# Kernel tuning notes

Measured on AMD Instinct MI355X. Metric: run time of the kernel, lower is better.

The kernel has to match this reference:

```python
import jax, jax.numpy as jnp
import numpy as np

N = 131072        # active input voxels (= output voxels for submanifold conv)
KVOL = 27         # 3x3x3 kernel volume
P = 65536         # neighbor pairs per kernel offset (regularized kernel map)
CIN = 64
COUT = 64


def setup_inputs() -> dict:
    key = jax.random.key(0)
    k1, k2, k3, k4, k5 = jax.random.split(key, 5)
    in_feats = jax.random.normal(k1, (N, CIN), dtype=jnp.float32)
    kernel = jax.random.normal(k2, (KVOL, CIN, COUT), dtype=jnp.float32) * (1.0 / np.sqrt(CIN * KVOL))
    bias_param = jax.random.normal(k3, (COUT,), dtype=jnp.float32)
    imap = jax.random.randint(k4, (KVOL, P), 0, N, dtype=jnp.int32)
    omap = jax.random.randint(k5, (KVOL, P), 0, N, dtype=jnp.int32)
    return {"in_feats": in_feats, "kernel": kernel, "bias_param": bias_param,
            "imap": imap, "omap": omap}


def reference(in_feats, kernel, bias_param, imap, omap):
    # Sparse 3D conv as gather -> per-offset GEMM -> scatter-add.
    # gathered: [KVOL, P, CIN]
    gathered = in_feats[imap]
    # per-offset GEMM: [KVOL, P, COUT]
    contrib = jnp.einsum('kpc,kco->kpo', gathered, kernel)
    out = jnp.zeros((N, COUT), dtype=in_feats.dtype)
    out = out.at[omap.reshape(-1)].add(contrib.reshape(-1, COUT))
    out = out + bias_param
    return out
```

## Files before the change

### kernel.cpp

```cpp
#include <hip/hip_runtime.h>
#include <hip/hip_bf16.h>
#include <stdint.h>

#define N_VOX 131072
#define KVOL  27
#define PPK   65536
#define CIN   64
#define COUT  64
#define TOT   (KVOL * PPK)
#define SORT_BLOCKS 864
#define GEMM_BLOCKS (KVOL * (PPK / 128))
#define NBUCKET 256
#define BUCKET_CAP 8192
#define CURSOR_STRIDE 16

typedef __attribute__((ext_vector_type(8))) short short8;
typedef __attribute__((ext_vector_type(4))) float f32x4;

__device__ __forceinline__ void gl_lds16(const void* g, void* l) {
  __builtin_amdgcn_global_load_lds(
      (const __attribute__((address_space(1))) unsigned int*)g,
      (__attribute__((address_space(3))) unsigned int*)l,
      16, 0, 0);
}

__device__ __forceinline__ unsigned short f2bf(float f) {
  __hip_bfloat16 h = __float2bfloat16(f);
  return *reinterpret_cast<unsigned short*>(&h);
}


__global__ __launch_bounds__(256) void prep_sort1_kernel(
    const float* __restrict__ in, unsigned short* __restrict__ inb,
    const float* __restrict__ w, unsigned short* __restrict__ wt,
    const int* __restrict__ omap, unsigned int* __restrict__ cursor,
    unsigned int* __restrict__ pairs, int do_sort) {
  int b = blockIdx.x;
  if (do_sort) {
    if (b < SORT_BLOCKS) {
      __shared__ unsigned int hist[NBUCKET];
      __shared__ unsigned int bbase[NBUCKET];
      int tid = threadIdx.x;
      hist[tid] = 0;
      __syncthreads();
      int e0 = (b * 256 + tid) * 8;
      int4 o0 = *(const int4*)(omap + e0);
      int4 o1 = *(const int4*)(omap + e0 + 4);
      unsigned int k[8] = {(unsigned)o0.x, (unsigned)o0.y, (unsigned)o0.z, (unsigned)o0.w,
                           (unsigned)o1.x, (unsigned)o1.y, (unsigned)o1.z, (unsigned)o1.w};
#pragma unroll
      for (int i = 0; i < 8; i++) atomicAdd(&hist[k[i] >> 9], 1u);
      __syncthreads();
      unsigned int n = hist[tid];
      unsigned int base = n ? atomicAdd(&cursor[tid * CURSOR_STRIDE], n) : 0u;
      bbase[tid] = (unsigned)tid * BUCKET_CAP + base;
      hist[tid] = 0;
      __syncthreads();
#pragma unroll
      for (int i = 0; i < 8; i++) {
        unsigned int bk = k[i] >> 9;
        unsigned int r = atomicAdd(&hist[bk], 1u);
        unsigned int pos = bbase[bk] + r;
        if (pos < (bk + 1) * BUCKET_CAP)
          pairs[pos] = (((unsigned)(e0 + i)) << 9) | (k[i] & 511u);
      }
      return;
    }
    b -= SORT_BLOCKS;
  }
  if (b < 4096) {
    int i = b * 256 + threadIdx.x;
    const float4* in4 = (const float4*)in;
    float4 f0 = in4[2 * i], f1 = in4[2 * i + 1];
    union { unsigned short u[8]; short8 v; } r;
    r.u[0] = f2bf(f0.x); r.u[1] = f2bf(f0.y); r.u[2] = f2bf(f0.z); r.u[3] = f2bf(f0.w);
    r.u[4] = f2bf(f1.x); r.u[5] = f2bf(f1.y); r.u[6] = f2bf(f1.z); r.u[7] = f2bf(f1.w);
    ((short8*)inb)[i] = r.v;
  } else {
    int k = b - 4096;
    const float* wk = w + k * CIN * COUT;
    unsigned short* wtk = wt + k * CIN * COUT;
    for (int idx = threadIdx.x; idx < CIN * COUT; idx += 256) {
      int c = idx >> 6, o = idx & 63;
      wtk[o * 64 + c] = f2bf(wk[idx]);
    }
  }
}


__global__ __launch_bounds__(512) void sort_pass2_kernel(
    const unsigned int* __restrict__ cursor, const unsigned int* __restrict__ pairs,
    int* __restrict__ islot, int* __restrict__ ofs, int* __restrict__ cnt) {
  __shared__ unsigned int hist[512];
  __shared__ unsigned int binofs[512];
  __shared__ unsigned int csc[512];
  __shared__ unsigned int sb_s, n_s;
  int b = blockIdx.x, tid = threadIdx.x;

  unsigned int cv = (tid < NBUCKET) ? cursor[tid * CURSOR_STRIDE] : 0u;
  csc[tid] = cv;
  __syncthreads();
  for (int off = 1; off < 512; off <<= 1) {
    unsigned int t = (tid >= off) ? csc[tid - off] : 0u;
    __syncthreads();
    csc[tid] += t;
    __syncthreads();
  }
  if (tid == b) {
    sb_s = csc[tid] - cv;
    n_s  = cv > BUCKET_CAP ? BUCKET_CAP : cv;
  }
  hist[tid] = 0;
  __syncthreads();
  unsigned int sb = sb_s, n = n_s;
  const unsigned int* reg = pairs + (size_t)b * BUCKET_CAP;

  for (unsigned int i = tid; i < n; i += 512)
    atomicAdd(&hist[reg[i] & 511u], 1u);
  __syncthreads();

  unsigned int h = hist[tid];
  csc[tid] = h;
  __syncthreads();
  for (int off = 1; off < 512; off <<= 1) {
    unsigned int t = (tid >= off) ? csc[tid - off] : 0u;
    __syncthreads();
    csc[tid] += t;
    __syncthreads();
  }
  binofs[tid] = csc[tid] - h;
  int key = (b << 9) | tid;
  ofs[key] = (int)(sb + binofs[tid]);
  cnt[key] = (int)h;
  __syncthreads();

  for (unsigned int i = tid; i < n; i += 512) {
    unsigned int v = reg[i];
    unsigned int r = atomicAdd(&binofs[v & 511u], 1u);
    islot[v >> 9] = (int)(sb + r);
  }
}


__global__ __launch_bounds__(256) void spconv_store_kernel(
    const unsigned short* __restrict__ inb,
    const unsigned short* __restrict__ wt,
    const int* __restrict__ imap,
    const int* __restrict__ islot,
    unsigned short* __restrict__ contrib) {
  __shared__ __align__(16) char smem[24576];
  short* A_lds = (short*)smem;
  short* B_lds = (short*)(smem + 16384);
  short* C_sh  = (short*)smem;
  __shared__ int perm_s[128];

  int bid = blockIdx.x;
  int k = bid >> 9;
  int pbase = (bid & 511) * 128;
  int tid = threadIdx.x;
  int wave = tid >> 6, lane = tid & 63;
  int m = lane & 15, q = lane >> 4;

  const int* imk = imap + k * PPK;
  const unsigned short* wtk = wt + k * 4096;

  if (tid < 128) perm_s[tid] = islot[k * PPK + pbase + tid];

#pragma unroll
  for (int i = 0; i < 2; i++) {
    int id = wave * 2 + i;
    int t = id >> 1, s = id & 1;
    const unsigned short* g = wtk + (t * 16 + m) * 64 + s * 32 + q * 8;
    gl_lds16(g, &B_lds[(t * 128 + s * 64) * 8]);
  }
#pragma unroll
  for (int j = 0; j < 2; j++) {
    int r = wave * 2 + j;
    int row = imk[pbase + r * 16 + m];
    const unsigned short* g0 = inb + row * 64 + q * 8;
    gl_lds16(g0,      &A_lds[(r * 128)      * 8]);
    gl_lds16(g0 + 32, &A_lds[(r * 128 + 64) * 8]);
  }
  __syncthreads();

  const short8* Af = (const short8*)A_lds;
  const short8* Bf = (const short8*)B_lds;

  short8 a[2][2], b[4][2];
#pragma unroll
  for (int r2 = 0; r2 < 2; r2++) {
    int r = wave * 2 + r2;
#pragma unroll
    for (int s = 0; s < 2; s++) a[r2][s] = Af[r * 128 + s * 64 + lane];
  }
#pragma unroll
  for (int t = 0; t < 4; t++)
#pragma unroll
    for (int s = 0; s < 2; s++) b[t][s] = Bf[t * 128 + s * 64 + lane];

  __syncthreads();

  f32x4 acc[2][4];
#pragma unroll
  for (int r2 = 0; r2 < 2; r2++)
#pragma unroll
    for (int t = 0; t < 4; t++) {
      f32x4 c = {0.f, 0.f, 0.f, 0.f};
      c = __builtin_amdgcn_mfma_f32_16x16x32_bf16(a[r2][0], b[t][0], c, 0, 0, 0);
      c = __builtin_amdgcn_mfma_f32_16x16x32_bf16(a[r2][1], b[t][1], c, 0, 0, 0);
      acc[r2][t] = c;
    }

#pragma unroll
  for (int r2 = 0; r2 < 2; r2++) {
    int pl = (wave * 2 + r2) * 16 + q * 4;
#pragma unroll
    for (int t = 0; t < 4; t++)
#pragma unroll
      for (int reg = 0; reg < 4; reg++)
        C_sh[(pl + reg) * 72 + t * 16 + m] = (short)f2bf(acc[r2][t][reg]);
  }
  __syncthreads();

#pragma unroll
  for (int i = 0; i < 4; i++) {
    int id = i * 256 + tid;
    int row = id >> 3, ch = (id & 7) * 8;
    short8 v = *(const short8*)&C_sh[row * 72 + ch];
    __builtin_nontemporal_store(v, (short8*)&contrib[(size_t)perm_s[row] * 64 + ch]);
  }
}


__global__ __launch_bounds__(256) void reduce_kernel(
    const unsigned short* __restrict__ contrib,
    const int* __restrict__ ofs,
    const int* __restrict__ cnt,
    const float* __restrict__ bias,
    float* __restrict__ out) {
  int row = blockIdx.x * 4 + (threadIdx.x >> 6);
  int lane = threadIdx.x & 63;
  int rg = lane >> 3, ch = (lane & 7) * 8;
  int s = ofs[row], n = cnt[row];

  float acc[8];
#pragma unroll
  for (int i = 0; i < 8; i++) acc[i] = 0.f;

  int j = rg;
  for (; j + 8 < n; j += 16) {
    short8 v0 = __builtin_nontemporal_load((const short8*)&contrib[(size_t)(s + j) * 64 + ch]);
    short8 v1 = __builtin_nontemporal_load((const short8*)&contrib[(size_t)(s + j + 8) * 64 + ch]);
#pragma unroll
    for (int i = 0; i < 8; i++)
      acc[i] += __uint_as_float((unsigned int)(unsigned short)v0[i] << 16);
#pragma unroll
    for (int i = 0; i < 8; i++)
      acc[i] += __uint_as_float((unsigned int)(unsigned short)v1[i] << 16);
  }
  if (j < n) {
    short8 v0 = __builtin_nontemporal_load((const short8*)&contrib[(size_t)(s + j) * 64 + ch]);
#pragma unroll
    for (int i = 0; i < 8; i++)
      acc[i] += __uint_as_float((unsigned int)(unsigned short)v0[i] << 16);
  }

#pragma unroll
  for (int mask = 8; mask < 64; mask <<= 1)
#pragma unroll
    for (int i = 0; i < 8; i++) acc[i] += __shfl_xor(acc[i], mask, 64);

  if (rg == 0) {
    float4 b0 = *(const float4*)(bias + ch);
    float4 b1 = *(const float4*)(bias + ch + 4);
    float4 r0 = {acc[0] + b0.x, acc[1] + b0.y, acc[2] + b0.z, acc[3] + b0.w};
    float4 r1 = {acc[4] + b1.x, acc[5] + b1.y, acc[6] + b1.z, acc[7] + b1.w};
    *(float4*)(out + (size_t)row * 64 + ch) = r0;
    *(float4*)(out + (size_t)row * 64 + ch + 4) = r1;
  }
}


__global__ __launch_bounds__(256) void init_out_kernel(float* __restrict__ out,
                                                       const float* __restrict__ bias) {
  int i = blockIdx.x * blockDim.x + threadIdx.x;
  float4 b = *(const float4*)(bias + ((i * 4) & 63));
  ((float4*)out)[i] = b;
}

__global__ __launch_bounds__(256) void spconv_atomic_kernel(
    const unsigned short* __restrict__ inb,
    const unsigned short* __restrict__ wt,
    const int* __restrict__ imap, const int* __restrict__ omap,
    float* __restrict__ out) {
  __shared__ __align__(16) short A_lds[128 * 64];
  __shared__ __align__(16) short B_lds[64 * 64];

  int bid = blockIdx.x;
  int k = bid >> 9;
  int pbase = (bid & 511) * 128;
  int tid = threadIdx.x;
  int wave = tid >> 6, lane = tid & 63;
  int m = lane & 15, q = lane >> 4;

  const int* imk = imap + k * PPK;
  const int* omk = omap + k * PPK;
  const unsigned short* wtk = wt + k * 4096;

#pragma unroll
  for (int i = 0; i < 2; i++) {
    int id = wave * 2 + i;
    int t = id >> 1, s = id & 1;
    const unsigned short* g = wtk + (t * 16 + m) * 64 + s * 32 + q * 8;
    gl_lds16(g, &B_lds[(t * 128 + s * 64) * 8]);
  }
#pragma unroll
  for (int j = 0; j < 2; j++) {
    int r = wave * 2 + j;
    int row = imk[pbase + r * 16 + m];
    const unsigned short* g0 = inb + row * 64 + q * 8;
    gl_lds16(g0,      &A_lds[(r * 128)      * 8]);
    gl_lds16(g0 + 32, &A_lds[(r * 128 + 64) * 8]);
  }
  __syncthreads();

  const short8* Af = (const short8*)A_lds;
  const short8* Bf = (const short8*)B_lds;
  short8 a[2][2], b[4][2];
#pragma unroll
  for (int r2 = 0; r2 < 2; r2++) {
    int r = wave * 2 + r2;
#pragma unroll
    for (int s = 0; s < 2; s++) a[r2][s] = Af[r * 128 + s * 64 + lane];
  }
#pragma unroll
  for (int t = 0; t < 4; t++)
#pragma unroll
    for (int s = 0; s < 2; s++) b[t][s] = Bf[t * 128 + s * 64 + lane];

  f32x4 acc[2][4];
#pragma unroll
  for (int r2 = 0; r2 < 2; r2++)
#pragma unroll
    for (int t = 0; t < 4; t++) {
      f32x4 c = {0.f, 0.f, 0.f, 0.f};
      c = __builtin_amdgcn_mfma_f32_16x16x32_bf16(a[r2][0], b[t][0], c, 0, 0, 0);
      c = __builtin_amdgcn_mfma_f32_16x16x32_bf16(a[r2][1], b[t][1], c, 0, 0, 0);
      acc[r2][t] = c;
    }

  int orow[2][4];
#pragma unroll
  for (int r2 = 0; r2 < 2; r2++) {
    int pr = pbase + (wave * 2 + r2) * 16 + q * 4;
#pragma unroll
    for (int reg = 0; reg < 4; reg++) orow[r2][reg] = omk[pr + reg];
  }
#pragma unroll
  for (int r2 = 0; r2 < 2; r2++)
#pragma unroll
    for (int t = 0; t < 4; t++)
#pragma unroll
      for (int reg = 0; reg < 4; reg++)
        atomicAdd(out + (size_t)orow[r2][reg] * 64 + t * 16 + m, acc[r2][t][reg]);
}


extern "C" void kernel_launch(void* const* d_in, const int* in_sizes, int n_in,
                              void* d_out, int out_size, void* d_ws, size_t ws_size,
                              hipStream_t stream) {
  const float* in_feats = (const float*)d_in[0];
  const float* kern     = (const float*)d_in[1];
  const float* bias     = (const float*)d_in[2];
  const int*   imap     = (const int*)d_in[3];
  const int*   omap     = (const int*)d_in[4];
  float* out = (float*)d_out;

  char* ws = (char*)d_ws;
  size_t off = 0;
  auto alloc = [&](size_t bytes) { size_t o = off; off = (off + bytes + 255) & ~(size_t)255; return o; };

  size_t o_inb   = alloc((size_t)N_VOX * CIN * 2);
  size_t o_wt    = alloc((size_t)KVOL * CIN * COUT * 2);
  size_t o_cnt   = alloc((size_t)N_VOX * 4);
  size_t o_ofs   = alloc((size_t)N_VOX * 4);
  size_t o_islot = alloc((size_t)TOT * 4);
  size_t o_cur   = alloc((size_t)NBUCKET * CURSOR_STRIDE * 4);
  size_t o_ctb   = alloc((size_t)TOT * 64 * 2);
  size_t needed = off;

  unsigned short* inb = (unsigned short*)(ws + o_inb);
  unsigned short* wt  = (unsigned short*)(ws + o_wt);
  int* cnt   = (int*)(ws + o_cnt);
  int* ofs   = (int*)(ws + o_ofs);
  int* islot = (int*)(ws + o_islot);
  unsigned int* cursor = (unsigned int*)(ws + o_cur);
  unsigned short* ctb = (unsigned short*)(ws + o_ctb);
  unsigned int* pairs = (unsigned int*)(ws + o_ctb);

  bool fast = (ws_size >= needed);

  if (fast) {
    (void)hipMemsetAsync(cursor, 0, (size_t)NBUCKET * CURSOR_STRIDE * 4, stream);
    prep_sort1_kernel<<<SORT_BLOCKS + 4096 + KVOL, 256, 0, stream>>>(
        in_feats, inb, kern, wt, omap, cursor, pairs, 1);
    sort_pass2_kernel<<<NBUCKET, 512, 0, stream>>>(cursor, pairs, islot, ofs, cnt);
    spconv_store_kernel<<<GEMM_BLOCKS, 256, 0, stream>>>(inb, wt, imap, islot, ctb);
    reduce_kernel<<<N_VOX / 4, 256, 0, stream>>>(ctb, ofs, cnt, bias, out);
  } else {
    prep_sort1_kernel<<<4096 + KVOL, 256, 0, stream>>>(
        in_feats, inb, kern, wt, omap, nullptr, nullptr, 0);
    init_out_kernel<<<(N_VOX * COUT / 4) / 256, 256, 0, stream>>>(out, bias);
    spconv_atomic_kernel<<<GEMM_BLOCKS, 256, 0, stream>>>(inb, wt, imap, omap, out);
  }
}
```

Measured before the change: 262.2 us.

## Replace two-pass bucket sort with partial counting sort and LDS-accumulating reduce

Replaces the atomic-cursor bucket sort and the per-voxel segmented second pass with a deterministic three-stage counting sort over 512 coarse buckets: per-block histograms, a scan, then a scatter that writes slot indices plus an 8-bit low key. The reduce now gives each block one 256-voxel bucket and accumulates contributions into a 64 KB LDS tile with shared-memory float atomics. This removes the global cursor atomics, the bucket-capacity limit and the fine-grained sort pass. The cost is extra kernel launches, 64 KB of LDS per reduce block (which limits occupancy), and only 512 reduce blocks.

```diff
diff --git a/kernel.cpp b/kernel.cpp
--- a/kernel.cpp
+++ b/kernel.cpp
@@ -10,9 +10,7 @@
 #define TOT   (KVOL * PPK)
 #define SORT_BLOCKS 864
 #define GEMM_BLOCKS (KVOL * (PPK / 128))
-#define NBUCKET 256
-#define BUCKET_CAP 8192
-#define CURSOR_STRIDE 16
+#define NB    512
 
 typedef __attribute__((ext_vector_type(8))) short short8;
 typedef __attribute__((ext_vector_type(4))) float f32x4;
@@ -30,40 +28,31 @@
 }
 
 
-__global__ __launch_bounds__(256) void prep_sort1_kernel(
+__global__ __launch_bounds__(256) void prep_hist_kernel(
     const float* __restrict__ in, unsigned short* __restrict__ inb,
     const float* __restrict__ w, unsigned short* __restrict__ wt,
-    const int* __restrict__ omap, unsigned int* __restrict__ cursor,
-    unsigned int* __restrict__ pairs, int do_sort) {
+    const int* __restrict__ omap, int* __restrict__ counts, int do_sort) {
   int b = blockIdx.x;
   if (do_sort) {
     if (b < SORT_BLOCKS) {
-      __shared__ unsigned int hist[NBUCKET];
-      __shared__ unsigned int bbase[NBUCKET];
+      __shared__ unsigned int hist[NB];
       int tid = threadIdx.x;
-      hist[tid] = 0;
+      hist[tid] = 0; hist[tid + 256] = 0;
       __syncthreads();
       int e0 = (b * 256 + tid) * 8;
       int4 o0 = *(const int4*)(omap + e0);
       int4 o1 = *(const int4*)(omap + e0 + 4);
-      unsigned int k[8] = {(unsigned)o0.x, (unsigned)o0.y, (unsigned)o0.z, (unsigned)o0.w,
-                           (unsigned)o1.x, (unsigned)o1.y, (unsigned)o1.z, (unsigned)o1.w};
-#pragma unroll
-      for (int i = 0; i < 8; i++) atomicAdd(&hist[k[i] >> 9], 1u);
+      atomicAdd(&hist[(unsigned)o0.x >> 8], 1u);
+      atomicAdd(&hist[(unsigned)o0.y >> 8], 1u);
+      atomicAdd(&hist[(unsigned)o0.z >> 8], 1u);
+      atomicAdd(&hist[(unsigned)o0.w >> 8], 1u);
+      atomicAdd(&hist[(unsigned)o1.x >> 8], 1u);
+      atomicAdd(&hist[(unsigned)o1.y >> 8], 1u);
+      atomicAdd(&hist[(unsigned)o1.z >> 8], 1u);
+      atomicAdd(&hist[(unsigned)o1.w >> 8], 1u);
       __syncthreads();
-      unsigned int n = hist[tid];
-      unsigned int base = n ? atomicAdd(&cursor[tid * CURSOR_STRIDE], n) : 0u;
-      bbase[tid] = (unsigned)tid * BUCKET_CAP + base;
-      hist[tid] = 0;
-      __syncthreads();
-#pragma unroll
-      for (int i = 0; i < 8; i++) {
-        unsigned int bk = k[i] >> 9;
-        unsigned int r = atomicAdd(&hist[bk], 1u);
-        unsigned int pos = bbase[bk] + r;
-        if (pos < (bk + 1) * BUCKET_CAP)
-          pairs[pos] = (((unsigned)(e0 + i)) << 9) | (k[i] & 511u);
-      }
+      counts[(size_t)tid * SORT_BLOCKS + b] = (int)hist[tid];
+      counts[(size_t)(tid + 256) * SORT_BLOCKS + b] = (int)hist[tid + 256];
       return;
     }
     b -= SORT_BLOCKS;
@@ -88,57 +77,80 @@
 }
 
 
-__global__ __launch_bounds__(512) void sort_pass2_kernel(
-    const unsigned int* __restrict__ cursor, const unsigned int* __restrict__ pairs,
-    int* __restrict__ islot, int* __restrict__ ofs, int* __restrict__ cnt) {
-  __shared__ unsigned int hist[512];
-  __shared__ unsigned int binofs[512];
-  __shared__ unsigned int csc[512];
-  __shared__ unsigned int sb_s, n_s;
+__global__ __launch_bounds__(256) void scan_blocks_kernel(
+    const int* __restrict__ counts, int* __restrict__ blockbase,
+    int* __restrict__ totals) {
+  __shared__ int s[256];
+  int b = blockIdx.x, t = threadIdx.x;
+  const int* row = counts + (size_t)b * SORT_BLOCKS;
+  int4 c = make_int4(0, 0, 0, 0);
+  if (t < 216) c = *(const int4*)(row + t * 4);
+  int sum = c.x + c.y + c.z + c.w;
+  s[t] = sum; __syncthreads();
+  for (int off = 1; off < 256; off <<= 1) {
+    int v = (t >= off) ? s[t - off] : 0;
+    __syncthreads();
+    s[t] += v;
+    __syncthreads();
+  }
+  int excl = s[t] - sum;
+  int* brow = blockbase + (size_t)b * SORT_BLOCKS;
+  if (t < 216) {
+    brow[t * 4]     = excl;
+    brow[t * 4 + 1] = excl + c.x;
+    brow[t * 4 + 2] = excl + c.x + c.y;
+    brow[t * 4 + 3] = excl + c.x + c.y + c.z;
+  }
+  if (t == 255) totals[b] = s[255];
+}
+
+
+__global__ __launch_bounds__(NB) void base_kernel(const int* __restrict__ totals,
+                                                  int* __restrict__ bbase) {
+  __shared__ int s[NB];
+  int t = threadIdx.x;
+  int v = totals[t];
+  s[t] = v; __syncthreads();
+  for (int off = 1; off < NB; off <<= 1) {
+    int x = (t >= off) ? s[t - off] : 0;
+    __syncthreads();
+    s[t] += x;
+    __syncthreads();
+  }
+  bbase[t] = s[t] - v;
+  if (t == NB - 1) bbase[NB] = s[NB - 1];
+}
+
+
+__global__ __launch_bounds__(256) void scatter_kernel(
+    const int* __restrict__ omap, const int* __restrict__ blockbase,
+    const int* __restrict__ bbase, int* __restrict__ islot,
+    unsigned char* __restrict__ lokey) {
+  __shared__ unsigned int gb[NB];
+  __shared__ unsigned int cur[NB];
   int b = blockIdx.x, tid = threadIdx.x;
-
-  unsigned int cv = (tid < NBUCKET) ? cursor[tid * CURSOR_STRIDE] : 0u;
-  csc[tid] = cv;
-  __syncthreads();
-  for (int off = 1; off < 512; off <<= 1) {
-    unsigned int t = (tid >= off) ? csc[tid - off] : 0u;
-    __syncthreads();
-    csc[tid] += t;
-    __syncthreads();
-  }
-  if (tid == b) {
-    sb_s = csc[tid] - cv;
-    n_s  = cv > BUCKET_CAP ? BUCKET_CAP : cv;
-  }
-  hist[tid] = 0;
-  __syncthreads();
-  unsigned int sb = sb_s, n = n_s;
-  const unsigned int* reg = pairs + (size_t)b * BUCKET_CAP;
-
-  for (unsigned int i = tid; i < n; i += 512)
-    atomicAdd(&hist[reg[i] & 511u], 1u);
-  __syncthreads();
-
-  unsigned int h = hist[tid];
-  csc[tid] = h;
-  __syncthreads();
-  for (int off = 1; off < 512; off <<= 1) {
-    unsigned int t = (tid >= off) ? csc[tid - off] : 0u;
-    __syncthreads();
-    csc[tid] += t;
-    __syncthreads();
-  }
-  binofs[tid] = csc[tid] - h;
-  int key = (b << 9) | tid;
-  ofs[key] = (int)(sb + binofs[tid]);
-  cnt[key] = (int)h;
-  __syncthreads();
-
-  for (unsigned int i = tid; i < n; i += 512) {
-    unsigned int v = reg[i];
-    unsigned int r = atomicAdd(&binofs[v & 511u], 1u);
-    islot[v >> 9] = (int)(sb + r);
-  }
+  for (int i = tid; i < NB; i += 256) {
+    gb[i] = (unsigned)(bbase[i] + blockbase[(size_t)i * SORT_BLOCKS + b]);
+    cur[i] = 0;
+  }
+  __syncthreads();
+  int e0 = (b * 256 + tid) * 8;
+  int4 o0 = *(const int4*)(omap + e0);
+  int4 o1 = *(const int4*)(omap + e0 + 4);
+  unsigned int key[8] = {(unsigned)o0.x, (unsigned)o0.y, (unsigned)o0.z, (unsigned)o0.w,
+                         (unsigned)o1.x, (unsigned)o1.y, (unsigned)o1.z, (unsigned)o1.w};
+  int res[8];
+#pragma unroll
+  for (int i = 0; i < 8; i++) {
+    unsigned int bk = key[i] >> 8;
+    unsigned int r = atomicAdd(&cur[bk], 1u);
+    unsigned int pos = gb[bk] + r;
+    unsigned int lo = key[i] & 255u;
+    res[i] = (int)((pos << 8) | lo);
+    lokey[pos] = (unsigned char)lo;
+  }
+  *(int4*)(islot + e0)     = make_int4(res[0], res[1], res[2], res[3]);
+  *(int4*)(islot + e0 + 4) = make_int4(res[4], res[5], res[6], res[7]);
 }
 
 
@@ -164,7 +176,7 @@
   const int* imk = imap + k * PPK;
   const unsigned short* wtk = wt + k * 4096;
 
-  if (tid < 128) perm_s[tid] = islot[k * PPK + pbase + tid];
+  if (tid < 128) perm_s[tid] = (int)(((unsigned)islot[k * PPK + pbase + tid]) >> 8);
 
 #pragma unroll
   for (int i = 0; i < 2; i++) {
@@ -232,51 +244,48 @@
 }
 
 
-__global__ __launch_bounds__(256) void reduce_kernel(
+__global__ __launch_bounds__(256) void reduce_lds_kernel(
     const unsigned short* __restrict__ contrib,
-    const int* __restrict__ ofs,
-    const int* __restrict__ cnt,
+    const unsigned char* __restrict__ lokey,
+    const int* __restrict__ bbase,
     const float* __restrict__ bias,
     float* __restrict__ out) {
-  int row = blockIdx.x * 4 + (threadIdx.x >> 6);
-  int lane = threadIdx.x & 63;
-  int rg = lane >> 3, ch = (lane & 7) * 8;
-  int s = ofs[row], n = cnt[row];
-
-  float acc[8];
-#pragma unroll
-  for (int i = 0; i < 8; i++) acc[i] = 0.f;
-
-  int j = rg;
-  for (; j + 8 < n; j += 16) {
-    short8 v0 = __builtin_nontemporal_load((const short8*)&contrib[(size_t)(s + j) * 64 + ch]);
-    short8 v1 = __builtin_nontemporal_load((const short8*)&contrib[(size_t)(s + j + 8) * 64 + ch]);
-#pragma unroll
-    for (int i = 0; i < 8; i++)
-      acc[i] += __uint_as_float((unsigned int)(unsigned short)v0[i] << 16);
-#pragma unroll
-    for (int i = 0; i < 8; i++)
-      acc[i] += __uint_as_float((unsigned int)(unsigned short)v1[i] << 16);
-  }
-  if (j < n) {
-    short8 v0 = __builtin_nontemporal_load((const short8*)&contrib[(size_t)(s + j) * 64 + ch]);
-#pragma unroll
-    for (int i = 0; i < 8; i++)
-      acc[i] += __uint_as_float((unsigned int)(unsigned short)v0[i] << 16);
-  }
-
-#pragma unroll
-  for (int mask = 8; mask < 64; mask <<= 1)
-#pragma unroll
-    for (int i = 0; i < 8; i++) acc[i] += __shfl_xor(acc[i], mask, 64);
-
-  if (rg == 0) {
-    float4 b0 = *(const float4*)(bias + ch);
-    float4 b1 = *(const float4*)(bias + ch + 4);
-    float4 r0 = {acc[0] + b0.x, acc[1] + b0.y, acc[2] + b0.z, acc[3] + b0.w};
-    float4 r1 = {acc[4] + b1.x, acc[5] + b1.y, acc[6] + b1.z, acc[7] + b1.w};
-    *(float4*)(out + (size_t)row * 64 + ch) = r0;
-    *(float4*)(out + (size_t)row * 64 + ch + 4) = r1;
+  __shared__ float acc[256 * 64];
+  int tid = threadIdx.x;
+  float4* a4 = (float4*)acc;
+#pragma unroll
+  for (int i = 0; i < 16; i++) a4[tid + i * 256] = make_float4(0.f, 0.f, 0.f, 0.f);
+  __syncthreads();
+
+  int b = blockIdx.x;
+  int sb = bbase[b], se = bbase[b + 1];
+  int w = tid >> 6, l = tid & 63;
+
+  int s = sb + w;
+  for (; s + 60 < se; s += 64) {
+    unsigned int v[16]; unsigned int kk[16];
+#pragma unroll
+    for (int u = 0; u < 16; u++) {
+      v[u]  = (unsigned int)__builtin_nontemporal_load(&contrib[(size_t)(s + 4 * u) * 64 + l]);
+      kk[u] = (unsigned int)lokey[s + 4 * u];
+    }
+#pragma unroll
+    for (int u = 0; u < 16; u++)
+      atomicAdd(&acc[kk[u] * 64 + l], __uint_as_float(v[u] << 16));
+  }
+  for (; s < se; s += 4) {
+    unsigned int v = (unsigned int)contrib[(size_t)s * 64 + l];
+    unsigned int kk = (unsigned int)lokey[s];
+    atomicAdd(&acc[kk * 64 + l], __uint_as_float(v << 16));
+  }
+  __syncthreads();
+
+  for (int j = tid; j < 4096; j += 256) {
+    int row = j >> 4, c4 = (j & 15) * 4;
+    float4 bb = *(const float4*)(bias + c4);
+    float4 a = a4[j];
+    float4 r = {a.x + bb.x, a.y + bb.y, a.z + bb.z, a.w + bb.w};
+    *(float4*)(out + ((size_t)b * 256 + row) * 64 + c4) = r;
   }
 }
 
@@ -382,34 +391,38 @@
 
   size_t o_inb   = alloc((size_t)N_VOX * CIN * 2);
   size_t o_wt    = alloc((size_t)KVOL * CIN * COUT * 2);
-  size_t o_cnt   = alloc((size_t)N_VOX * 4);
-  size_t o_ofs   = alloc((size_t)N_VOX * 4);
+  size_t o_cts   = alloc((size_t)NB * SORT_BLOCKS * 4);
+  size_t o_bb    = alloc((size_t)NB * SORT_BLOCKS * 4);
+  size_t o_tot   = alloc((size_t)NB * 4);
+  size_t o_bbase = alloc((size_t)(NB + 1) * 4);
   size_t o_islot = alloc((size_t)TOT * 4);
-  size_t o_cur   = alloc((size_t)NBUCKET * CURSOR_STRIDE * 4);
+  size_t o_lok   = alloc((size_t)TOT);
   size_t o_ctb   = alloc((size_t)TOT * 64 * 2);
   size_t needed = off;
 
   unsigned short* inb = (unsigned short*)(ws + o_inb);
   unsigned short* wt  = (unsigned short*)(ws + o_wt);
-  int* cnt   = (int*)(ws + o_cnt);
-  int* ofs   = (int*)(ws + o_ofs);
-  int* islot = (int*)(ws + o_islot);
-  unsigned int* cursor = (unsigned int*)(ws + o_cur);
-  unsigned short* ctb = (unsigned short*)(ws + o_ctb);
-  unsigned int* pairs = (unsigned int*)(ws + o_ctb);
+  int* counts    = (int*)(ws + o_cts);
+  int* blockbase = (int*)(ws + o_bb);
+  int* totals    = (int*)(ws + o_tot);
+  int* bbase     = (int*)(ws + o_bbase);
+  int* islot     = (int*)(ws + o_islot);
+  unsigned char* lokey = (unsigned char*)(ws + o_lok);
+  unsigned short* ctb  = (unsigned short*)(ws + o_ctb);
 
   bool fast = (ws_size >= needed);
 
   if (fast) {
-    (void)hipMemsetAsync(cursor, 0, (size_t)NBUCKET * CURSOR_STRIDE * 4, stream);
-    prep_sort1_kernel<<<SORT_BLOCKS + 4096 + KVOL, 256, 0, stream>>>(
-        in_feats, inb, kern, wt, omap, cursor, pairs, 1);
-    sort_pass2_kernel<<<NBUCKET, 512, 0, stream>>>(cursor, pairs, islot, ofs, cnt);
+    prep_hist_kernel<<<SORT_BLOCKS + 4096 + KVOL, 256, 0, stream>>>(
+        in_feats, inb, kern, wt, omap, counts, 1);
+    scan_blocks_kernel<<<NB, 256, 0, stream>>>(counts, blockbase, totals);
+    base_kernel<<<1, NB, 0, stream>>>(totals, bbase);
+    scatter_kernel<<<SORT_BLOCKS, 256, 0, stream>>>(omap, blockbase, bbase, islot, lokey);
     spconv_store_kernel<<<GEMM_BLOCKS, 256, 0, stream>>>(inb, wt, imap, islot, ctb);
-    reduce_kernel<<<N_VOX / 4, 256, 0, stream>>>(ctb, ofs, cnt, bias, out);
+    reduce_lds_kernel<<<NB, 256, 0, stream>>>(ctb, lokey, bbase, bias, out);
   } else {
-    prep_sort1_kernel<<<4096 + KVOL, 256, 0, stream>>>(
-        in_feats, inb, kern, wt, omap, nullptr, nullptr, 0);
+    prep_hist_kernel<<<4096 + KVOL, 256, 0, stream>>>(
+        in_feats, inb, kern, wt, omap, nullptr, 0);
     init_out_kernel<<<(N_VOX * COUT / 4) / 256, 256, 0, stream>>>(out, bias);
     spconv_atomic_kernel<<<GEMM_BLOCKS, 256, 0, stream>>>(inb, wt, imap, omap, out);
   }
```

Result: slower. 762.9 us (+191.0%).
